# Kernel optimization log

Hardware: AMD Instinct MI355X
Metric: run time of the kernel (lower is better)

## Reference

```python
import jax, jax.numpy as jnp
import numpy as np

K = 32        # num_classes
NQ = 16384    # num query samples
C = 512       # feature_dim
H_REF = 512   # refinement_net hidden
H_CONF = 256  # confidence_net hidden
NUM_STEPS = 3


def setup_inputs() -> dict:
    key = jax.random.key(0)
    ks = jax.random.split(key, 8)
    s = 0.02
    return {
        "prototypes": jax.random.normal(ks[0], (K, C), jnp.float32),
        "query_features": jax.random.normal(ks[1], (NQ, C), jnp.float32),
        "query_distances": jax.random.uniform(ks[2], (NQ, K), jnp.float32) * 10.0,
        "W1": jax.random.normal(ks[3], (2 * C, H_REF), jnp.float32) * s,
        "b1": jnp.zeros((H_REF,), jnp.float32),
        "W2": jax.random.normal(ks[4], (H_REF, C), jnp.float32) * s,
        "b2": jnp.zeros((C,), jnp.float32),
        "Wc1": jax.random.normal(ks[5], (2 * C, H_CONF), jnp.float32) * s,
        "bc1": jnp.zeros((H_CONF,), jnp.float32),
        "Wc2": jax.random.normal(ks[6], (H_CONF, 1), jnp.float32) * s,
        "bc2": jnp.zeros((1,), jnp.float32),
    }


def reference(prototypes, query_features, query_distances,
              W1, b1, W2, b2, Wc1, bc1, Wc2, bc2):
    # ---- refinement loop (3 steps, sequential in refined prototypes) ----
    refined = prototypes
    for step in range(NUM_STEPS):
        # soft assignments over classes; temperature = step + 1
        soft = jax.nn.softmax(-query_distances / (step + 1.0), axis=-1)  # (NQ, K)
        wsum = jnp.maximum(soft.sum(axis=0), 1e-6)                       # (K,)  clamp(min=1e-6)
        wmean = (soft.T @ query_features) / wsum[:, None]                # (K, C)
        concat = jnp.concatenate([refined, wmean], axis=-1)              # (K, 2C)
        h = jax.nn.relu(concat @ W1 + b1)                                # dropout is identity in eval
        refinement = h @ W2 + b2                                         # (K, C)
        refined = refined + 0.1 * refinement

    # ---- confidence scores: MLP on [proto, query] pairs, mean over queries ----
    # Split first-layer weight into proto half and query half to avoid
    # materializing the (K, NQ, 2C) concat explicitly (same math).
    Wp, Wq = Wc1[:C], Wc1[C:]
    hp = prototypes @ Wp          # (K, H_CONF)
    hq = query_features @ Wq      # (NQ, H_CONF)
    hidden = jax.nn.relu(hp[:, None, :] + hq[None, :, :] + bc1)  # (K, NQ, H_CONF)
    conf = jax.nn.sigmoid(hidden @ Wc2 + bc2)                    # (K, NQ, 1)
    confidence_scores = conf.reshape(K, -1).mean(axis=1)         # (K,)

    return refined, confidence_scores
```

## Files before the change

kernel.cpp:

```cpp
#include <hip/hip_runtime.h>

#define KP 32
#define NQg 16384
#define CD 512
#define HC 256
#define NS 3

typedef __attribute__((ext_vector_type(8))) short short8;
typedef __attribute__((ext_vector_type(4))) short short4_t;
typedef __attribute__((ext_vector_type(8))) __bf16 bf16x8;
typedef __attribute__((ext_vector_type(4))) float floatx4;

union S8B8 { short8 s; bf16x8 b; };

__device__ __forceinline__ short f2bf(float f) {
    union { float f; unsigned u; } v; v.f = f;
    unsigned r = v.u + 0x7fffu + ((v.u >> 16) & 1u);
    return (short)(r >> 16);
}
__device__ __forceinline__ float bf2f(short s) {
    union { unsigned u; float f; } v; v.u = ((unsigned)(unsigned short)s) << 16;
    return v.f;
}
__device__ __forceinline__ float bflo(unsigned u) { return __uint_as_float(u << 16); }
__device__ __forceinline__ float bfhi(unsigned u) { return __uint_as_float(u & 0xffff0000u); }

__global__ __launch_bounds__(256) void k_A(const float* __restrict__ qd,
                                           const float* __restrict__ W1, const float* __restrict__ W2,
                                           const float* __restrict__ Wc1, const float* __restrict__ proto,
                                           const float* __restrict__ qf,
                                           short* __restrict__ softT,
                                           short* __restrict__ W1p, short* __restrict__ W2p,
                                           short* __restrict__ wqp, float* __restrict__ refined,
                                           short* __restrict__ qf2b, float* __restrict__ wmean,
                                           int* __restrict__ bar, float* __restrict__ dout) {
    int tid = threadIdx.x;
    int bid = blockIdx.x;
    if (bid < 64) {
        int q = bid * 256 + tid;
        float d[32];
        const float4* p = (const float4*)(qd + (size_t)q * 32);
#pragma unroll
        for (int j = 0; j < 8; j++) {
            float4 v = p[j];
            d[4 * j] = v.x; d[4 * j + 1] = v.y; d[4 * j + 2] = v.z; d[4 * j + 3] = v.w;
        }
#pragma unroll
        for (int s = 0; s < 3; s++) {
            float inv = -1.0f / (float)(s + 1);
            float e[32];
            float sum = 0.f;
#pragma unroll
            for (int k = 0; k < 32; k++) { e[k] = __expf(d[k] * inv); sum += e[k]; }
            float r = 1.0f / sum;
#pragma unroll
            for (int k = 0; k < 32; k++)
                softT[(size_t)(s * 32 + k) * NQg + q] = f2bf(e[k] * r);
        }
        return;
    }
    if (bid < 3712) {
        if (bid == 64) {
            if (tid < 32) dout[16384 + tid] = 0.f;
            else if (tid < 40) bar[tid - 32] = 0;
        }
        int idx = (bid - 64) * 256 + tid;
        if (idx < 524288) {
            int k = idx >> 9, n = idx & 511;
            W1p[((size_t)(k >> 3) * 512 + n) * 8 + (k & 7)] = f2bf(W1[idx]);
        } else if (idx < 786432) {
            int j = idx - 524288;
            int k = j >> 9, n = j & 511;
            W2p[((size_t)(k >> 3) * 512 + n) * 8 + (k & 7)] = f2bf(W2[j]);
        } else if (idx < 917504) {
            int j = idx - 786432;
            int k = j >> 8, n = j & 255;
            wqp[((size_t)(k >> 3) * 256 + n) * 8 + (k & 7)] = f2bf(Wc1[(size_t)(512 + k) * 256 + n]);
        } else {
            int j = idx - 917504;
            refined[j] = proto[j];
        }
        return;
    }
    if (bid < 3904) {
        int idx = (bid - 3712) * 256 + tid;
        wmean[idx] = 0.f;
        return;
    }
    {
#pragma unroll
        for (int it = 0; it < 4; it++) {
            int j = (bid - 3904) * 1024 + it * 256 + tid;
            float4 v = *(const float4*)&qf[(size_t)j * 4];
            short4_t o;
            o[0] = f2bf(v.x); o[1] = f2bf(v.y); o[2] = f2bf(v.z); o[3] = f2bf(v.w);
            *(short4_t*)&qf2b[(size_t)j * 4] = o;
        }
    }
}

__global__ __launch_bounds__(256) void k_B(const short* __restrict__ qf2b,
                                           const short* __restrict__ softT,
                                           const short* __restrict__ wqp,
                                           float* __restrict__ wmean,
                                           short* __restrict__ hq_g,
                                           float* __restrict__ wsuminv,
                                           const float* __restrict__ proto,
                                           const float* __restrict__ Wc1,
                                           const float* __restrict__ bc1,
                                           float* __restrict__ hpb) {
    __shared__ short B_lds[128 * 40];
    int tid = threadIdx.x;
    int lane = tid & 63, w = tid >> 6;
    int ml = lane & 15, q8 = lane >> 4;

    if (blockIdx.x < 256) {
        int kc = blockIdx.x >> 2, ns = blockIdx.x & 3;
        int c0 = ns * 128;
        int qbase0 = kc * 256;
        int c_l = 2 * lane;
        int q_l = 8 * w;

        floatx4 acc[6][2];
#pragma unroll
        for (int mt = 0; mt < 6; mt++)
#pragma unroll
            for (int nt = 0; nt < 2; nt++) acc[mt][nt] = (floatx4){0.f, 0.f, 0.f, 0.f};

        for (int step = 0; step < 8; step++) {
            int qb = qbase0 + step * 32;
            short8 sA, sB;
#pragma unroll
            for (int i = 0; i < 8; i++) {
                unsigned u = *(const unsigned*)&qf2b[(size_t)(qb + q_l + i) * 512 + c0 + c_l];
                sA[i] = (short)(u & 0xffffu);
                sB[i] = (short)(u >> 16);
            }
            __syncthreads();
            *(short8*)&B_lds[c_l * 40 + q_l] = sA;
            *(short8*)&B_lds[(c_l + 1) * 40 + q_l] = sB;
            S8B8 a[6];
#pragma unroll
            for (int mt = 0; mt < 6; mt++)
                a[mt].s = *(const short8*)&softT[(size_t)(mt * 16 + ml) * NQg + qb + q8 * 8];
            __syncthreads();
#pragma unroll
            for (int nt = 0; nt < 2; nt++) {
                S8B8 b; b.s = *(short8*)&B_lds[(w * 32 + nt * 16 + ml) * 40 + q8 * 8];
#pragma unroll
                for (int mt = 0; mt < 6; mt++)
                    acc[mt][nt] = __builtin_amdgcn_mfma_f32_16x16x32_bf16(a[mt].b, b.b, acc[mt][nt], 0, 0, 0);
            }
        }
#pragma unroll
        for (int mt = 0; mt < 6; mt++) {
#pragma unroll
            for (int nt = 0; nt < 2; nt++) {
                int c = c0 + w * 32 + nt * 16 + ml;
#pragma unroll
                for (int r = 0; r < 4; r++) {
                    int m = mt * 16 + q8 * 4 + r;
                    atomicAdd(&wmean[(size_t)m * 512 + c], acc[mt][nt][r]);
                }
            }
        }
    } else if (blockIdx.x < 512) {
        int m0 = (blockIdx.x - 256) * 64;
        int n0 = w * 64;
        floatx4 acc[4][4];
#pragma unroll
        for (int mt = 0; mt < 4; mt++)
#pragma unroll
            for (int nt = 0; nt < 4; nt++) acc[mt][nt] = (floatx4){0.f, 0.f, 0.f, 0.f};

#pragma unroll 4
        for (int kc = 0; kc < 512; kc += 32) {
            S8B8 a[4], b[4];
#pragma unroll
            for (int mt = 0; mt < 4; mt++)
                a[mt].s = *(const short8*)&qf2b[(size_t)(m0 + mt * 16 + ml) * 512 + kc + q8 * 8];
#pragma unroll
            for (int nt = 0; nt < 4; nt++)
                b[nt].s = *(const short8*)&wqp[((size_t)((kc >> 3) + q8) * 256 + n0 + nt * 16 + ml) * 8];
#pragma unroll
            for (int mt = 0; mt < 4; mt++)
#pragma unroll
                for (int nt = 0; nt < 4; nt++)
                    acc[mt][nt] = __builtin_amdgcn_mfma_f32_16x16x32_bf16(a[mt].b, b[nt].b, acc[mt][nt], 0, 0, 0);
        }
#pragma unroll
        for (int mt = 0; mt < 4; mt++)
#pragma unroll
            for (int nt = 0; nt < 4; nt++) {
                int col = n0 + nt * 16 + ml;
#pragma unroll
                for (int r = 0; r < 4; r++) {
                    int row = m0 + mt * 16 + q8 * 4 + r;
                    hq_g[(size_t)row * 256 + col] = f2bf(acc[mt][nt][r]);
                }
            }
    } else if (blockIdx.x < 608) {
        float* red = (float*)B_lds;
        int sk = blockIdx.x - 512;
        const short* row = softT + (size_t)sk * NQg;
        float s = 0.f;
#pragma unroll
        for (int j = 0; j < 8; j++) {
            short8 v = *(const short8*)&row[j * 2048 + tid * 8];
#pragma unroll
            for (int i = 0; i < 8; i++) s += bf2f(v[i]);
        }
        red[tid] = s;
        __syncthreads();
        for (int off = 128; off > 0; off >>= 1) {
            if (tid < off) red[tid] += red[tid + off];
            __syncthreads();
        }
        if (tid == 0) wsuminv[sk] = 1.0f / fmaxf(red[0], 1e-6f);
    } else {
        int r = blockIdx.x - 608;
        const float* pr = proto + r * 512;
        const float* wc = Wc1 + tid;
        float a0 = 0.f, a1 = 0.f, a2 = 0.f, a3 = 0.f;
#pragma unroll 4
        for (int i = 0; i < 512; i += 4) {
            float4 p4 = *(const float4*)&pr[i];
            float w0 = wc[(size_t)i * 256];
            float w1 = wc[(size_t)(i + 1) * 256];
            float w2 = wc[(size_t)(i + 2) * 256];
            float w3 = wc[(size_t)(i + 3) * 256];
            a0 += p4.x * w0;
            a1 += p4.y * w1;
            a2 += p4.z * w2;
            a3 += p4.w * w3;
        }
        hpb[r * 256 + tid] = bc1[tid] + ((a0 + a1) + (a2 + a3));
    }
}

__device__ __forceinline__ void gbar(int* bar, int phase, int nblk) {
    __syncthreads();
    if (threadIdx.x == 0) {
        __threadfence();
        __hip_atomic_fetch_add(&bar[phase], 1, __ATOMIC_ACQ_REL, __HIP_MEMORY_SCOPE_AGENT);
        while (__hip_atomic_load(&bar[phase], __ATOMIC_ACQUIRE, __HIP_MEMORY_SCOPE_AGENT) < nblk)
            __builtin_amdgcn_s_sleep(1);
    }
    __syncthreads();
}

__global__ __launch_bounds__(256) void k_D(const float* __restrict__ wmean,
                                           const float* __restrict__ wsuminv,
                                           const short* __restrict__ W1p,
                                           const float* __restrict__ b1,
                                           const short* __restrict__ W2p,
                                           const float* __restrict__ b2,
                                           float* __restrict__ refined,
                                           short* __restrict__ hb,
                                           int* __restrict__ bar,
                                           const short* __restrict__ hq_g,
                                           const float* __restrict__ hpb,
                                           const float* __restrict__ Wc2,
                                           const float* __restrict__ bc2p,
                                           float* __restrict__ dout) {
    __shared__ float smem[6688];
    int tid = threadIdx.x, lane = tid & 63, w = tid >> 6;
    int ml = lane & 15, q8 = lane >> 4;

    if (blockIdx.x < 16) {
        float (*red)[32][36] = (float(*)[32][36])smem;
        int nb = blockIdx.x;
        int phase = 0;
        for (int s = 0; s < 3; s++) {
            {
                const float* srcA = (w < 2) ? refined : (wmean + (size_t)s * 32 * 512 - 512);
                float iv0 = 1.f, iv1 = 1.f;
                if (w >= 2) {
                    iv0 = wsuminv[s * 32 + ml];
                    iv1 = wsuminv[s * 32 + 16 + ml];
                }
                int kw = w * 256;
                floatx4 acc[2][2];
#pragma unroll
                for (int mt = 0; mt < 2; mt++)
#pragma unroll
                    for (int nt = 0; nt < 2; nt++) acc[mt][nt] = (floatx4){0.f, 0.f, 0.f, 0.f};
                for (int st = 0; st < 8; st++) {
                    int k0 = kw + st * 32 + q8 * 8;
                    S8B8 a[2];
#pragma unroll
                    for (int mt = 0; mt < 2; mt++) {
                        float sc = mt ? iv1 : iv0;
                        const float* p = &srcA[(size_t)(mt * 16 + ml) * 512 + k0];
                        float4 f0 = *(const float4*)p;
                        float4 f1 = *(const float4*)(p + 4);
                        short8 t;
                        t[0] = f2bf(f0.x * sc); t[1] = f2bf(f0.y * sc);
                        t[2] = f2bf(f0.z * sc); t[3] = f2bf(f0.w * sc);
                        t[4] = f2bf(f1.x * sc); t[5] = f2bf(f1.y * sc);
                        t[6] = f2bf(f1.z * sc); t[7] = f2bf(f1.w * sc);
                        a[mt].s = t;
                    }
#pragma unroll
                    for (int nt = 0; nt < 2; nt++) {
                        int n = nb * 32 + nt * 16 + ml;
                        S8B8 b; b.s = *(const short8*)&W1p[((size_t)(k0 >> 3) * 512 + n) * 8];
#pragma unroll
                        for (int mt = 0; mt < 2; mt++)
                            acc[mt][nt] = __builtin_amdgcn_mfma_f32_16x16x32_bf16(a[mt].b, b.b, acc[mt][nt], 0, 0, 0);
                    }
                }
                __syncthreads();
#pragma unroll
                for (int mt = 0; mt < 2; mt++)
#pragma unroll
                    for (int nt = 0; nt < 2; nt++)
#pragma unroll
                        for (int r = 0; r < 4; r++)
                            red[w][mt * 16 + q8 * 4 + r][nt * 16 + ml] = acc[mt][nt][r];
                __syncthreads();
                int m = tid >> 3, n0 = (tid & 7) * 4;
                short4_t o;
#pragma unroll
                for (int i = 0; i < 4; i++) {
                    float v = b1[nb * 32 + n0 + i];
#pragma unroll
                    for (int w4 = 0; w4 < 4; w4++) v += red[w4][m][n0 + i];
                    o[i] = f2bf(fmaxf(v, 0.f));
                }
                *(short4_t*)&hb[(size_t)m * 512 + nb * 32 + n0] = o;
            }
            gbar(bar, phase++, 16);
            {
                int kw = w * 128;
                floatx4 acc[2][2];
#pragma unroll
                for (int mt = 0; mt < 2; mt++)
#pragma unroll
                    for (int nt = 0; nt < 2; nt++) acc[mt][nt] = (floatx4){0.f, 0.f, 0.f, 0.f};
                for (int st = 0; st < 4; st++) {
                    int k0 = kw + st * 32 + q8 * 8;
                    S8B8 a[2];
#pragma unroll
                    for (int mt = 0; mt < 2; mt++)
                        a[mt].s = *(const short8*)&hb[(size_t)(mt * 16 + ml) * 512 + k0];
#pragma unroll
                    for (int nt = 0; nt < 2; nt++) {
                        int n = nb * 32 + nt * 16 + ml;
                        S8B8 b; b.s = *(const short8*)&W2p[((size_t)(k0 >> 3) * 512 + n) * 8];
#pragma unroll
                        for (int mt = 0; mt < 2; mt++)
                            acc[mt][nt] = __builtin_amdgcn_mfma_f32_16x16x32_bf16(a[mt].b, b.b, acc[mt][nt], 0, 0, 0);
                    }
                }
                __syncthreads();
#pragma unroll
                for (int mt = 0; mt < 2; mt++)
#pragma unroll
                    for (int nt = 0; nt < 2; nt++)
#pragma unroll
                        for (int r = 0; r < 4; r++)
                            red[w][mt * 16 + q8 * 4 + r][nt * 16 + ml] = acc[mt][nt][r];
                __syncthreads();
                int m = tid >> 3, n0 = (tid & 7) * 4;
#pragma unroll
                for (int i = 0; i < 4; i++) {
                    int c = nb * 32 + n0 + i;
                    float v = b2[c];
#pragma unroll
                    for (int w4 = 0; w4 < 4; w4++) v += red[w4][m][n0 + i];
                    float val = refined[(size_t)m * 512 + c] + 0.1f * v;
                    refined[(size_t)m * 512 + c] = val;
                    if (s == 2) dout[(size_t)m * 512 + c] = val;
                }
            }
            if (s < 2) gbar(bar, phase++, 16);
        }
    } else {
        short* hq_lds = (short*)smem;
        short* hp_s   = (short*)smem + 4480;
        float* wc2s   = smem + 6400;
        float* confl  = smem + 6656;
        int q0 = (blockIdx.x - 16) * 16;

        wc2s[tid] = Wc2[tid];
        if (tid < 32) confl[tid] = 0.f;
#pragma unroll
        for (int i = 0; i < 8; i++) {
            int idx = i * 256 + tid;
            int r = idx >> 6, c = (idx & 63) * 4;
            float4 v = *(const float4*)&hpb[r * 256 + c];
            short4_t o;
            o[0] = f2bf(v.x); o[1] = f2bf(v.y); o[2] = f2bf(v.z); o[3] = f2bf(v.w);
            *(short4_t*)&hp_s[r * 260 + c] = o;
        }
        {
            const short* hqs = hq_g + (size_t)q0 * 256;
            int r = tid >> 4, c = (tid & 15) * 16;
            *(short8*)&hq_lds[r * 280 + c] = *(const short8*)&hqs[r * 256 + c];
            *(short8*)&hq_lds[r * 280 + c + 8] = *(const short8*)&hqs[r * 256 + c + 8];
        }
        __syncthreads();

        int q = tid & 15, kg = tid >> 4;
        int k0 = kg, k1 = kg + 16;
        float s0 = 0.f, s1 = 0.f;
        for (int h = 0; h < 256; h += 4) {
            uint2 hv = *(uint2*)&hq_lds[q * 280 + h];
            float f0 = bflo(hv.x), f1 = bfhi(hv.x), f2 = bflo(hv.y), f3 = bfhi(hv.y);
            uint2 u0 = *(uint2*)&hp_s[k0 * 260 + h];
            uint2 u1 = *(uint2*)&hp_s[k1 * 260 + h];
            float4 wv = *(float4*)&wc2s[h];
            s0 += fmaxf(bflo(u0.x) + f0, 0.f) * wv.x;
            s0 += fmaxf(bfhi(u0.x) + f1, 0.f) * wv.y;
            s0 += fmaxf(bflo(u0.y) + f2, 0.f) * wv.z;
            s0 += fmaxf(bfhi(u0.y) + f3, 0.f) * wv.w;
            s1 += fmaxf(bflo(u1.x) + f0, 0.f) * wv.x;
            s1 += fmaxf(bfhi(u1.x) + f1, 0.f) * wv.y;
            s1 += fmaxf(bflo(u1.y) + f2, 0.f) * wv.z;
            s1 += fmaxf(bfhi(u1.y) + f3, 0.f) * wv.w;
        }
        float bc2 = bc2p[0];
        float v0 = 1.f / (1.f + __expf(-(s0 + bc2)));
        float v1 = 1.f / (1.f + __expf(-(s1 + bc2)));
        atomicAdd(&confl[k0], v0);
        atomicAdd(&confl[k1], v1);
        __syncthreads();
        if (tid < 32) atomicAdd(&dout[16384 + tid], confl[tid] * (1.0f / 16384.0f));
    }
}

extern "C" void kernel_launch(void* const* d_in, const int* in_sizes, int n_in,
                              void* d_out, int out_size, void* d_ws, size_t ws_size,
                              hipStream_t stream) {
    const float* proto = (const float*)d_in[0];
    const float* qf    = (const float*)d_in[1];
    const float* qd    = (const float*)d_in[2];
    const float* W1    = (const float*)d_in[3];
    const float* b1    = (const float*)d_in[4];
    const float* W2    = (const float*)d_in[5];
    const float* b2    = (const float*)d_in[6];
    const float* Wc1   = (const float*)d_in[7];
    const float* bc1   = (const float*)d_in[8];
    const float* Wc2   = (const float*)d_in[9];
    const float* bc2   = (const float*)d_in[10];
    float* out = (float*)d_out;

    float* ws = (float*)d_ws;
    short* softT   = (short*)ws;
    short* qf2b    = (short*)(ws + 786432);
    float* wmean   = ws + 4980736;
    float* refined = ws + 5029888;
    short* hb      = (short*)(ws + 5046272);
    short* W1p     = (short*)(ws + 5054464);
    short* W2p     = (short*)(ws + 5316608);
    short* wqp     = (short*)(ws + 5447680);
    float* hpb     = ws + 5513216;
    int*   bar     = (int*)(ws + 5521408);
    float* wsuminv = ws + 5521416;
    short* hq      = (short*)(ws + 5521536);

    k_A<<<5952, 256, 0, stream>>>(qd, W1, W2, Wc1, proto, qf, softT, W1p, W2p, wqp,
                                  refined, qf2b, wmean, bar, out);
    k_B<<<640, 256, 0, stream>>>(qf2b, softT, wqp, wmean, hq, wsuminv, proto, Wc1, bc1, hpb);
    k_D<<<1040, 256, 0, stream>>>(wmean, wsuminv, W1p, b1, W2p, b2, refined, hb, bar,
                                  hq, hpb, Wc2, bc2, out);
}
```

Baseline: 172.8 us.

## Fuse hq GEMM into confidence blocks and regroup kernels across stages

Removes the separate hq GEMM and its global round-trip. Each confidence block now computes its 16-row slice of query_features @ Wq with MFMA directly into LDS. The hp projection moves into the prep kernel, and weight packing writes eight bf16 values per thread as one vector store. The confidence work now runs in the second kernel alongside the wmean reduction, leaving the third kernel as only the 16-block sequential refinement loop. Atomic targets are rotated to spread contention, at the cost of redundant reads of the Wq weights across many blocks.

```diff
diff --git a/kernel.cpp b/kernel.cpp
--- a/kernel.cpp
+++ b/kernel.cpp
@@ -1,10 +1,6 @@
 #include <hip/hip_runtime.h>
 
-#define KP 32
 #define NQg 16384
-#define CD 512
-#define HC 256
-#define NS 3
 
 typedef __attribute__((ext_vector_type(8))) short short8;
 typedef __attribute__((ext_vector_type(4))) short short4_t;
@@ -28,14 +24,14 @@
 __global__ __launch_bounds__(256) void k_A(const float* __restrict__ qd,
                                            const float* __restrict__ W1, const float* __restrict__ W2,
                                            const float* __restrict__ Wc1, const float* __restrict__ proto,
-                                           const float* __restrict__ qf,
+                                           const float* __restrict__ qf, const float* __restrict__ bc1,
                                            short* __restrict__ softT,
                                            short* __restrict__ W1p, short* __restrict__ W2p,
                                            short* __restrict__ wqp, float* __restrict__ refined,
                                            short* __restrict__ qf2b, float* __restrict__ wmean,
+                                           float* __restrict__ hpb,
                                            int* __restrict__ bar, float* __restrict__ dout) {
-    int tid = threadIdx.x;
-    int bid = blockIdx.x;
+    int tid = threadIdx.x, bid = blockIdx.x;
     if (bid < 64) {
         int q = bid * 256 + tid;
         float d[32];
@@ -59,166 +55,54 @@
         }
         return;
     }
-    if (bid < 3712) {
-        if (bid == 64) {
-            if (tid < 32) dout[16384 + tid] = 0.f;
-            else if (tid < 40) bar[tid - 32] = 0;
-        }
+    if (bid < 512) {
         int idx = (bid - 64) * 256 + tid;
-        if (idx < 524288) {
-            int k = idx >> 9, n = idx & 511;
-            W1p[((size_t)(k >> 3) * 512 + n) * 8 + (k & 7)] = f2bf(W1[idx]);
-        } else if (idx < 786432) {
-            int j = idx - 524288;
-            int k = j >> 9, n = j & 511;
-            W2p[((size_t)(k >> 3) * 512 + n) * 8 + (k & 7)] = f2bf(W2[j]);
-        } else if (idx < 917504) {
-            int j = idx - 786432;
-            int k = j >> 8, n = j & 255;
-            wqp[((size_t)(k >> 3) * 256 + n) * 8 + (k & 7)] = f2bf(Wc1[(size_t)(512 + k) * 256 + n]);
+        if (idx < 65536) {
+            int kg = idx >> 9, n = idx & 511;
+            short8 o;
+#pragma unroll
+            for (int j = 0; j < 8; j++) o[j] = f2bf(W1[(size_t)(kg * 8 + j) * 512 + n]);
+            *(short8*)&W1p[((size_t)kg * 512 + n) * 8] = o;
+        } else if (idx < 98304) {
+            int j2 = idx - 65536;
+            int kg = j2 >> 9, n = j2 & 511;
+            short8 o;
+#pragma unroll
+            for (int j = 0; j < 8; j++) o[j] = f2bf(W2[(size_t)(kg * 8 + j) * 512 + n]);
+            *(short8*)&W2p[((size_t)kg * 512 + n) * 8] = o;
         } else {
-            int j = idx - 917504;
-            refined[j] = proto[j];
-        }
-        return;
-    }
-    if (bid < 3904) {
-        int idx = (bid - 3712) * 256 + tid;
+            int j3 = idx - 98304;
+            int kg = j3 >> 8, n = j3 & 255;
+            short8 o;
+#pragma unroll
+            for (int j = 0; j < 8; j++) o[j] = f2bf(Wc1[(size_t)(512 + kg * 8 + j) * 256 + n]);
+            *(short8*)&wqp[((size_t)kg * 256 + n) * 8] = o;
+        }
+        return;
+    }
+    if (bid < 576) {
+        int idx = (bid - 512) * 256 + tid;
+        refined[idx] = proto[idx];
+        return;
+    }
+    if (bid < 768) {
+        int idx = (bid - 576) * 256 + tid;
         wmean[idx] = 0.f;
         return;
     }
-    {
+    if (bid < 2816) {
 #pragma unroll
         for (int it = 0; it < 4; it++) {
-            int j = (bid - 3904) * 1024 + it * 256 + tid;
+            int j = (bid - 768) * 1024 + it * 256 + tid;
             float4 v = *(const float4*)&qf[(size_t)j * 4];
             short4_t o;
             o[0] = f2bf(v.x); o[1] = f2bf(v.y); o[2] = f2bf(v.z); o[3] = f2bf(v.w);
             *(short4_t*)&qf2b[(size_t)j * 4] = o;
         }
-    }
-}
-
-__global__ __launch_bounds__(256) void k_B(const short* __restrict__ qf2b,
-                                           const short* __restrict__ softT,
-                                           const short* __restrict__ wqp,
-                                           float* __restrict__ wmean,
-                                           short* __restrict__ hq_g,
-                                           float* __restrict__ wsuminv,
-                                           const float* __restrict__ proto,
-                                           const float* __restrict__ Wc1,
-                                           const float* __restrict__ bc1,
-                                           float* __restrict__ hpb) {
-    __shared__ short B_lds[128 * 40];
-    int tid = threadIdx.x;
-    int lane = tid & 63, w = tid >> 6;
-    int ml = lane & 15, q8 = lane >> 4;
-
-    if (blockIdx.x < 256) {
-        int kc = blockIdx.x >> 2, ns = blockIdx.x & 3;
-        int c0 = ns * 128;
-        int qbase0 = kc * 256;
-        int c_l = 2 * lane;
-        int q_l = 8 * w;
-
-        floatx4 acc[6][2];
-#pragma unroll
-        for (int mt = 0; mt < 6; mt++)
-#pragma unroll
-            for (int nt = 0; nt < 2; nt++) acc[mt][nt] = (floatx4){0.f, 0.f, 0.f, 0.f};
-
-        for (int step = 0; step < 8; step++) {
-            int qb = qbase0 + step * 32;
-            short8 sA, sB;
-#pragma unroll
-            for (int i = 0; i < 8; i++) {
-                unsigned u = *(const unsigned*)&qf2b[(size_t)(qb + q_l + i) * 512 + c0 + c_l];
-                sA[i] = (short)(u & 0xffffu);
-                sB[i] = (short)(u >> 16);
-            }
-            __syncthreads();
-            *(short8*)&B_lds[c_l * 40 + q_l] = sA;
-            *(short8*)&B_lds[(c_l + 1) * 40 + q_l] = sB;
-            S8B8 a[6];
-#pragma unroll
-            for (int mt = 0; mt < 6; mt++)
-                a[mt].s = *(const short8*)&softT[(size_t)(mt * 16 + ml) * NQg + qb + q8 * 8];
-            __syncthreads();
-#pragma unroll
-            for (int nt = 0; nt < 2; nt++) {
-                S8B8 b; b.s = *(short8*)&B_lds[(w * 32 + nt * 16 + ml) * 40 + q8 * 8];
-#pragma unroll
-                for (int mt = 0; mt < 6; mt++)
-                    acc[mt][nt] = __builtin_amdgcn_mfma_f32_16x16x32_bf16(a[mt].b, b.b, acc[mt][nt], 0, 0, 0);
-            }
-        }
-#pragma unroll
-        for (int mt = 0; mt < 6; mt++) {
-#pragma unroll
-            for (int nt = 0; nt < 2; nt++) {
-                int c = c0 + w * 32 + nt * 16 + ml;
-#pragma unroll
-                for (int r = 0; r < 4; r++) {
-                    int m = mt * 16 + q8 * 4 + r;
-                    atomicAdd(&wmean[(size_t)m * 512 + c], acc[mt][nt][r]);
-                }
-            }
-        }
-    } else if (blockIdx.x < 512) {
-        int m0 = (blockIdx.x - 256) * 64;
-        int n0 = w * 64;
-        floatx4 acc[4][4];
-#pragma unroll
-        for (int mt = 0; mt < 4; mt++)
-#pragma unroll
-            for (int nt = 0; nt < 4; nt++) acc[mt][nt] = (floatx4){0.f, 0.f, 0.f, 0.f};
-
-#pragma unroll 4
-        for (int kc = 0; kc < 512; kc += 32) {
-            S8B8 a[4], b[4];
-#pragma unroll
-            for (int mt = 0; mt < 4; mt++)
-                a[mt].s = *(const short8*)&qf2b[(size_t)(m0 + mt * 16 + ml) * 512 + kc + q8 * 8];
-#pragma unroll
-            for (int nt = 0; nt < 4; nt++)
-                b[nt].s = *(const short8*)&wqp[((size_t)((kc >> 3) + q8) * 256 + n0 + nt * 16 + ml) * 8];
-#pragma unroll
-            for (int mt = 0; mt < 4; mt++)
-#pragma unroll
-                for (int nt = 0; nt < 4; nt++)
-                    acc[mt][nt] = __builtin_amdgcn_mfma_f32_16x16x32_bf16(a[mt].b, b[nt].b, acc[mt][nt], 0, 0, 0);
-        }
-#pragma unroll
-        for (int mt = 0; mt < 4; mt++)
-#pragma unroll
-            for (int nt = 0; nt < 4; nt++) {
-                int col = n0 + nt * 16 + ml;
-#pragma unroll
-                for (int r = 0; r < 4; r++) {
-                    int row = m0 + mt * 16 + q8 * 4 + r;
-                    hq_g[(size_t)row * 256 + col] = f2bf(acc[mt][nt][r]);
-                }
-            }
-    } else if (blockIdx.x < 608) {
-        float* red = (float*)B_lds;
-        int sk = blockIdx.x - 512;
-        const short* row = softT + (size_t)sk * NQg;
-        float s = 0.f;
-#pragma unroll
-        for (int j = 0; j < 8; j++) {
-            short8 v = *(const short8*)&row[j * 2048 + tid * 8];
-#pragma unroll
-            for (int i = 0; i < 8; i++) s += bf2f(v[i]);
-        }
-        red[tid] = s;
-        __syncthreads();
-        for (int off = 128; off > 0; off >>= 1) {
-            if (tid < off) red[tid] += red[tid + off];
-            __syncthreads();
-        }
-        if (tid == 0) wsuminv[sk] = 1.0f / fmaxf(red[0], 1e-6f);
-    } else {
-        int r = blockIdx.x - 608;
+        return;
+    }
+    if (bid < 2848) {
+        int r = bid - 2816;
         const float* pr = proto + r * 512;
         const float* wc = Wc1 + tid;
         float a0 = 0.f, a1 = 0.f, a2 = 0.f, a3 = 0.f;
@@ -235,153 +119,106 @@
             a3 += p4.w * w3;
         }
         hpb[r * 256 + tid] = bc1[tid] + ((a0 + a1) + (a2 + a3));
-    }
-}
-
-__device__ __forceinline__ void gbar(int* bar, int phase, int nblk) {
-    __syncthreads();
-    if (threadIdx.x == 0) {
-        __threadfence();
-        __hip_atomic_fetch_add(&bar[phase], 1, __ATOMIC_ACQ_REL, __HIP_MEMORY_SCOPE_AGENT);
-        while (__hip_atomic_load(&bar[phase], __ATOMIC_ACQUIRE, __HIP_MEMORY_SCOPE_AGENT) < nblk)
-            __builtin_amdgcn_s_sleep(1);
-    }
-    __syncthreads();
-}
-
-__global__ __launch_bounds__(256) void k_D(const float* __restrict__ wmean,
-                                           const float* __restrict__ wsuminv,
-                                           const short* __restrict__ W1p,
-                                           const float* __restrict__ b1,
-                                           const short* __restrict__ W2p,
-                                           const float* __restrict__ b2,
-                                           float* __restrict__ refined,
-                                           short* __restrict__ hb,
-                                           int* __restrict__ bar,
-                                           const short* __restrict__ hq_g,
+        return;
+    }
+    {
+        if (tid < 8) bar[tid] = 0;
+        else if (tid >= 32 && tid < 64) dout[16384 + tid - 32] = 0.f;
+    }
+}
+
+__global__ __launch_bounds__(256) void k_B(const short* __restrict__ qf2b,
+                                           const short* __restrict__ softT,
+                                           float* __restrict__ wmean,
+                                           float* __restrict__ wsuminv,
+                                           const short* __restrict__ wqp,
                                            const float* __restrict__ hpb,
                                            const float* __restrict__ Wc2,
                                            const float* __restrict__ bc2p,
                                            float* __restrict__ dout) {
     __shared__ float smem[6688];
-    int tid = threadIdx.x, lane = tid & 63, w = tid >> 6;
+    int tid = threadIdx.x;
+    int lane = tid & 63, w = tid >> 6;
     int ml = lane & 15, q8 = lane >> 4;
-
-    if (blockIdx.x < 16) {
-        float (*red)[32][36] = (float(*)[32][36])smem;
-        int nb = blockIdx.x;
-        int phase = 0;
-        for (int s = 0; s < 3; s++) {
-            {
-                const float* srcA = (w < 2) ? refined : (wmean + (size_t)s * 32 * 512 - 512);
-                float iv0 = 1.f, iv1 = 1.f;
-                if (w >= 2) {
-                    iv0 = wsuminv[s * 32 + ml];
-                    iv1 = wsuminv[s * 32 + 16 + ml];
+    int bid = blockIdx.x;
+
+    if (bid < 256) {
+        short* B_lds = (short*)smem;
+        int kc = bid >> 2, ns = bid & 3;
+        int c0 = ns * 128;
+        int qbase0 = kc * 256;
+        int c_l = 2 * lane;
+        int q_l = 8 * w;
+
+        floatx4 acc[6][2];
+#pragma unroll
+        for (int mt = 0; mt < 6; mt++)
+#pragma unroll
+            for (int nt = 0; nt < 2; nt++) acc[mt][nt] = (floatx4){0.f, 0.f, 0.f, 0.f};
+
+        for (int step = 0; step < 8; step++) {
+            int qb = qbase0 + step * 32;
+            short8 sA, sB;
+#pragma unroll
+            for (int i = 0; i < 8; i++) {
+                unsigned u = *(const unsigned*)&qf2b[(size_t)(qb + q_l + i) * 512 + c0 + c_l];
+                sA[i] = (short)(u & 0xffffu);
+                sB[i] = (short)(u >> 16);
+            }
+            __syncthreads();
+            *(short8*)&B_lds[c_l * 40 + q_l] = sA;
+            *(short8*)&B_lds[(c_l + 1) * 40 + q_l] = sB;
+            S8B8 a[6];
+#pragma unroll
+            for (int mt = 0; mt < 6; mt++)
+                a[mt].s = *(const short8*)&softT[(size_t)(mt * 16 + ml) * NQg + qb + q8 * 8];
+            __syncthreads();
+#pragma unroll
+            for (int nt = 0; nt < 2; nt++) {
+                S8B8 b; b.s = *(short8*)&B_lds[(w * 32 + nt * 16 + ml) * 40 + q8 * 8];
+#pragma unroll
+                for (int mt = 0; mt < 6; mt++)
+                    acc[mt][nt] = __builtin_amdgcn_mfma_f32_16x16x32_bf16(a[mt].b, b.b, acc[mt][nt], 0, 0, 0);
+            }
+        }
+        int mrot = kc % 6;
+#pragma unroll
+        for (int mtt = 0; mtt < 6; mtt++) {
+            int mt = mtt + mrot; if (mt >= 6) mt -= 6;
+#pragma unroll
+            for (int nt = 0; nt < 2; nt++) {
+                int c = c0 + w * 32 + nt * 16 + ml;
+#pragma unroll
+                for (int r = 0; r < 4; r++) {
+                    int m = mt * 16 + q8 * 4 + r;
+                    atomicAdd(&wmean[(size_t)m * 512 + c], acc[mt][nt][r]);
                 }
-                int kw = w * 256;
-                floatx4 acc[2][2];
-#pragma unroll
-                for (int mt = 0; mt < 2; mt++)
-#pragma unroll
-                    for (int nt = 0; nt < 2; nt++) acc[mt][nt] = (floatx4){0.f, 0.f, 0.f, 0.f};
-                for (int st = 0; st < 8; st++) {
-                    int k0 = kw + st * 32 + q8 * 8;
-                    S8B8 a[2];
-#pragma unroll
-                    for (int mt = 0; mt < 2; mt++) {
-                        float sc = mt ? iv1 : iv0;
-                        const float* p = &srcA[(size_t)(mt * 16 + ml) * 512 + k0];
-                        float4 f0 = *(const float4*)p;
-                        float4 f1 = *(const float4*)(p + 4);
-                        short8 t;
-                        t[0] = f2bf(f0.x * sc); t[1] = f2bf(f0.y * sc);
-                        t[2] = f2bf(f0.z * sc); t[3] = f2bf(f0.w * sc);
-                        t[4] = f2bf(f1.x * sc); t[5] = f2bf(f1.y * sc);
-                        t[6] = f2bf(f1.z * sc); t[7] = f2bf(f1.w * sc);
-                        a[mt].s = t;
-                    }
-#pragma unroll
-                    for (int nt = 0; nt < 2; nt++) {
-                        int n = nb * 32 + nt * 16 + ml;
-                        S8B8 b; b.s = *(const short8*)&W1p[((size_t)(k0 >> 3) * 512 + n) * 8];
-#pragma unroll
-                        for (int mt = 0; mt < 2; mt++)
-                            acc[mt][nt] = __builtin_amdgcn_mfma_f32_16x16x32_bf16(a[mt].b, b.b, acc[mt][nt], 0, 0, 0);
-                    }
-                }
-                __syncthreads();
-#pragma unroll
-                for (int mt = 0; mt < 2; mt++)
-#pragma unroll
-                    for (int nt = 0; nt < 2; nt++)
-#pragma unroll
-                        for (int r = 0; r < 4; r++)
-                            red[w][mt * 16 + q8 * 4 + r][nt * 16 + ml] = acc[mt][nt][r];
-                __syncthreads();
-                int m = tid >> 3, n0 = (tid & 7) * 4;
-                short4_t o;
-#pragma unroll
-                for (int i = 0; i < 4; i++) {
-                    float v = b1[nb * 32 + n0 + i];
-#pragma unroll
-                    for (int w4 = 0; w4 < 4; w4++) v += red[w4][m][n0 + i];
-                    o[i] = f2bf(fmaxf(v, 0.f));
-                }
-                *(short4_t*)&hb[(size_t)m * 512 + nb * 32 + n0] = o;
-            }
-            gbar(bar, phase++, 16);
-            {
-                int kw = w * 128;
-                floatx4 acc[2][2];
-#pragma unroll
-                for (int mt = 0; mt < 2; mt++)
-#pragma unroll
-                    for (int nt = 0; nt < 2; nt++) acc[mt][nt] = (floatx4){0.f, 0.f, 0.f, 0.f};
-                for (int st = 0; st < 4; st++) {
-                    int k0 = kw + st * 32 + q8 * 8;
-                    S8B8 a[2];
-#pragma unroll
-                    for (int mt = 0; mt < 2; mt++)
-                        a[mt].s = *(const short8*)&hb[(size_t)(mt * 16 + ml) * 512 + k0];
-#pragma unroll
-                    for (int nt = 0; nt < 2; nt++) {
-                        int n = nb * 32 + nt * 16 + ml;
-                        S8B8 b; b.s = *(const short8*)&W2p[((size_t)(k0 >> 3) * 512 + n) * 8];
-#pragma unroll
-                        for (int mt = 0; mt < 2; mt++)
-                            acc[mt][nt] = __builtin_amdgcn_mfma_f32_16x16x32_bf16(a[mt].b, b.b, acc[mt][nt], 0, 0, 0);
-                    }
-                }
-                __syncthreads();
-#pragma unroll
-                for (int mt = 0; mt < 2; mt++)
-#pragma unroll
-                    for (int nt = 0; nt < 2; nt++)
-#pragma unroll
-                        for (int r = 0; r < 4; r++)
-                            red[w][mt * 16 + q8 * 4 + r][nt * 16 + ml] = acc[mt][nt][r];
-                __syncthreads();
-                int m = tid >> 3, n0 = (tid & 7) * 4;
-#pragma unroll
-                for (int i = 0; i < 4; i++) {
-                    int c = nb * 32 + n0 + i;
-                    float v = b2[c];
-#pragma unroll
-                    for (int w4 = 0; w4 < 4; w4++) v += red[w4][m][n0 + i];
-                    float val = refined[(size_t)m * 512 + c] + 0.1f * v;
-                    refined[(size_t)m * 512 + c] = val;
-                    if (s == 2) dout[(size_t)m * 512 + c] = val;
-                }
-            }
-            if (s < 2) gbar(bar, phase++, 16);
-        }
+            }
+        }
+    } else if (bid < 352) {
+        float* red = smem;
+        int sk = bid - 256;
+        const short* row = softT + (size_t)sk * NQg;
+        float s = 0.f;
+#pragma unroll
+        for (int j = 0; j < 8; j++) {
+            short8 v = *(const short8*)&row[j * 2048 + tid * 8];
+#pragma unroll
+            for (int i = 0; i < 8; i++) s += bf2f(v[i]);
+        }
+        red[tid] = s;
+        __syncthreads();
+        for (int off = 128; off > 0; off >>= 1) {
+            if (tid < off) red[tid] += red[tid + off];
+            __syncthreads();
+        }
+        if (tid == 0) wsuminv[sk] = 1.0f / fmaxf(red[0], 1e-6f);
     } else {
         short* hq_lds = (short*)smem;
         short* hp_s   = (short*)smem + 4480;
         float* wc2s   = smem + 6400;
         float* confl  = smem + 6656;
-        int q0 = (blockIdx.x - 16) * 16;
+        int q0 = (bid - 352) * 16;
 
         wc2s[tid] = Wc2[tid];
         if (tid < 32) confl[tid] = 0.f;
@@ -395,10 +232,25 @@
             *(short4_t*)&hp_s[r * 260 + c] = o;
         }
         {
-            const short* hqs = hq_g + (size_t)q0 * 256;
-            int r = tid >> 4, c = (tid & 15) * 16;
-            *(short8*)&hq_lds[r * 280 + c] = *(const short8*)&hqs[r * 256 + c];
-            *(short8*)&hq_lds[r * 280 + c + 8] = *(const short8*)&hqs[r * 256 + c + 8];
+            floatx4 acc[4];
+#pragma unroll
+            for (int nt = 0; nt < 4; nt++) acc[nt] = (floatx4){0.f, 0.f, 0.f, 0.f};
+            const short* qa = qf2b + (size_t)(q0 + ml) * 512 + q8 * 8;
+#pragma unroll 4
+            for (int kc = 0; kc < 512; kc += 32) {
+                S8B8 a; a.s = *(const short8*)&qa[kc];
+#pragma unroll
+                for (int nt = 0; nt < 4; nt++) {
+                    int col = w * 64 + nt * 16 + ml;
+                    S8B8 b; b.s = *(const short8*)&wqp[((size_t)((kc >> 3) + q8) * 256 + col) * 8];
+                    acc[nt] = __builtin_amdgcn_mfma_f32_16x16x32_bf16(a.b, b.b, acc[nt], 0, 0, 0);
+                }
+            }
+#pragma unroll
+            for (int nt = 0; nt < 4; nt++)
+#pragma unroll
+                for (int r = 0; r < 4; r++)
+                    hq_lds[(q8 * 4 + r) * 280 + w * 64 + nt * 16 + ml] = f2bf(acc[nt][r]);
         }
         __syncthreads();
 
@@ -426,7 +278,145 @@
         atomicAdd(&confl[k0], v0);
         atomicAdd(&confl[k1], v1);
         __syncthreads();
-        if (tid < 32) atomicAdd(&dout[16384 + tid], confl[tid] * (1.0f / 16384.0f));
+        if (tid < 32) {
+            int cell = (tid + bid) & 31;
+            atomicAdd(&dout[16384 + cell], confl[cell] * (1.0f / 16384.0f));
+        }
+    }
+}
+
+__device__ __forceinline__ void gbar(int* bar, int phase, int nblk) {
+    __syncthreads();
+    if (threadIdx.x == 0) {
+        __threadfence();
+        __hip_atomic_fetch_add(&bar[phase], 1, __ATOMIC_ACQ_REL, __HIP_MEMORY_SCOPE_AGENT);
+        while (__hip_atomic_load(&bar[phase], __ATOMIC_ACQUIRE, __HIP_MEMORY_SCOPE_AGENT) < nblk)
+            __builtin_amdgcn_s_sleep(1);
+    }
+    __syncthreads();
+}
+
+__global__ __launch_bounds__(256) void k_D(const float* __restrict__ wmean,
+                                           const float* __restrict__ wsuminv,
+                                           const short* __restrict__ W1p,
+                                           const float* __restrict__ b1,
+                                           const short* __restrict__ W2p,
+                                           const float* __restrict__ b2,
+                                           float* __restrict__ refined,
+                                           short* __restrict__ hb,
+                                           int* __restrict__ bar,
+                                           float* __restrict__ dout) {
+    __shared__ float smem[4608];
+    int tid = threadIdx.x, lane = tid & 63, w = tid >> 6;
+    int ml = lane & 15, q8 = lane >> 4;
+
+    float (*red)[32][36] = (float(*)[32][36])smem;
+    int nb = blockIdx.x;
+    int phase = 0;
+    for (int s = 0; s < 3; s++) {
+        {
+            const float* srcA = (w < 2) ? refined : (wmean + (size_t)s * 32 * 512 - 512);
+            float iv0 = 1.f, iv1 = 1.f;
+            if (w >= 2) {
+                iv0 = wsuminv[s * 32 + ml];
+                iv1 = wsuminv[s * 32 + 16 + ml];
+            }
+            int kw = w * 256;
+            floatx4 acc[2][2];
+#pragma unroll
+            for (int mt = 0; mt < 2; mt++)
+#pragma unroll
+                for (int nt = 0; nt < 2; nt++) acc[mt][nt] = (floatx4){0.f, 0.f, 0.f, 0.f};
+            for (int st = 0; st < 8; st++) {
+                int k0 = kw + st * 32 + q8 * 8;
+                S8B8 a[2];
+#pragma unroll
+                for (int mt = 0; mt < 2; mt++) {
+                    float sc = mt ? iv1 : iv0;
+                    const float* p = &srcA[(size_t)(mt * 16 + ml) * 512 + k0];
+                    float4 f0 = *(const float4*)p;
+                    float4 f1 = *(const float4*)(p + 4);
+                    short8 t;
+                    t[0] = f2bf(f0.x * sc); t[1] = f2bf(f0.y * sc);
+                    t[2] = f2bf(f0.z * sc); t[3] = f2bf(f0.w * sc);
+                    t[4] = f2bf(f1.x * sc); t[5] = f2bf(f1.y * sc);
+                    t[6] = f2bf(f1.z * sc); t[7] = f2bf(f1.w * sc);
+                    a[mt].s = t;
+                }
+#pragma unroll
+                for (int nt = 0; nt < 2; nt++) {
+                    int n = nb * 32 + nt * 16 + ml;
+                    S8B8 b; b.s = *(const short8*)&W1p[((size_t)(k0 >> 3) * 512 + n) * 8];
+#pragma unroll
+                    for (int mt = 0; mt < 2; mt++)
+                        acc[mt][nt] = __builtin_amdgcn_mfma_f32_16x16x32_bf16(a[mt].b, b.b, acc[mt][nt], 0, 0, 0);
+                }
+            }
+            __syncthreads();
+#pragma unroll
+            for (int mt = 0; mt < 2; mt++)
+#pragma unroll
+                for (int nt = 0; nt < 2; nt++)
+#pragma unroll
+                    for (int r = 0; r < 4; r++)
+                        red[w][mt * 16 + q8 * 4 + r][nt * 16 + ml] = acc[mt][nt][r];
+            __syncthreads();
+            int m = tid >> 3, n0 = (tid & 7) * 4;
+            short4_t o;
+#pragma unroll
+            for (int i = 0; i < 4; i++) {
+                float v = b1[nb * 32 + n0 + i];
+#pragma unroll
+                for (int w4 = 0; w4 < 4; w4++) v += red[w4][m][n0 + i];
+                o[i] = f2bf(fmaxf(v, 0.f));
+            }
+            *(short4_t*)&hb[(size_t)m * 512 + nb * 32 + n0] = o;
+        }
+        gbar(bar, phase++, 16);
+        {
+            int kw = w * 128;
+            floatx4 acc[2][2];
+#pragma unroll
+            for (int mt = 0; mt < 2; mt++)
+#pragma unroll
+                for (int nt = 0; nt < 2; nt++) acc[mt][nt] = (floatx4){0.f, 0.f, 0.f, 0.f};
+            for (int st = 0; st < 4; st++) {
+                int k0 = kw + st * 32 + q8 * 8;
+                S8B8 a[2];
+#pragma unroll
+                for (int mt = 0; mt < 2; mt++)
+                    a[mt].s = *(const short8*)&hb[(size_t)(mt * 16 + ml) * 512 + k0];
+#pragma unroll
+                for (int nt = 0; nt < 2; nt++) {
+                    int n = nb * 32 + nt * 16 + ml;
+                    S8B8 b; b.s = *(const short8*)&W2p[((size_t)(k0 >> 3) * 512 + n) * 8];
+#pragma unroll
+                    for (int mt = 0; mt < 2; mt++)
+                        acc[mt][nt] = __builtin_amdgcn_mfma_f32_16x16x32_bf16(a[mt].b, b.b, acc[mt][nt], 0, 0, 0);
+                }
+            }
+            __syncthreads();
+#pragma unroll
+            for (int mt = 0; mt < 2; mt++)
+#pragma unroll
+                for (int nt = 0; nt < 2; nt++)
+#pragma unroll
+                    for (int r = 0; r < 4; r++)
+                        red[w][mt * 16 + q8 * 4 + r][nt * 16 + ml] = acc[mt][nt][r];
+            __syncthreads();
+            int m = tid >> 3, n0 = (tid & 7) * 4;
+#pragma unroll
+            for (int i = 0; i < 4; i++) {
+                int c = nb * 32 + n0 + i;
+                float v = b2[c];
+#pragma unroll
+                for (int w4 = 0; w4 < 4; w4++) v += red[w4][m][n0 + i];
+                float val = refined[(size_t)m * 512 + c] + 0.1f * v;
+                refined[(size_t)m * 512 + c] = val;
+                if (s == 2) dout[(size_t)m * 512 + c] = val;
+            }
+        }
+        if (s < 2) gbar(bar, phase++, 16);
     }
 }
 
@@ -458,11 +448,9 @@
     float* hpb     = ws + 5513216;
     int*   bar     = (int*)(ws + 5521408);
     float* wsuminv = ws + 5521416;
-    short* hq      = (short*)(ws + 5521536);
-
-    k_A<<<5952, 256, 0, stream>>>(qd, W1, W2, Wc1, proto, qf, softT, W1p, W2p, wqp,
-                                  refined, qf2b, wmean, bar, out);
-    k_B<<<640, 256, 0, stream>>>(qf2b, softT, wqp, wmean, hq, wsuminv, proto, Wc1, bc1, hpb);
-    k_D<<<1040, 256, 0, stream>>>(wmean, wsuminv, W1p, b1, W2p, b2, refined, hb, bar,
-                                  hq, hpb, Wc2, bc2, out);
-}
+
+    k_A<<<2849, 256, 0, stream>>>(qd, W1, W2, Wc1, proto, qf, bc1, softT, W1p, W2p, wqp,
+                                  refined, qf2b, wmean, hpb, bar, out);
+    k_B<<<1376, 256, 0, stream>>>(qf2b, softT, wmean, wsuminv, wqp, hpb, Wc2, bc2, out);
+    k_D<<<16, 256, 0, stream>>>(wmean, wsuminv, W1p, b1, W2p, b2, refined, hb, bar, out);
+}
```

After: 200.7 us. 1.16x slower.
